# Kernel optimization log

Measured on AMD Instinct MI355X. Metric: run time of the kernel, lower is better.

Reference implementation:

```python
import jax, jax.numpy as jnp
import numpy as np

B, SEQ, DIM, HEADS = 2, 2048, 512, 8
HD = DIM // HEADS
RANK, DFF = 128, 1024
TAU_MEM, TAU_ADAPT, SLOPE, EPS = 0.99, 0.95, 25.0, 1e-6
THRESH, ADAPT_STRENGTH = 0.5, 0.1
TREE_LEVELS = int(np.log2(SEQ))  # 11


def rmsnorm(x, w, eps=EPS):
    return x * jax.lax.rsqrt(jnp.mean(x * x, axis=-1, keepdims=True) + eps) * w


def rope_cos_sin(seq, hd):
    inv = 1.0 / (10000.0 ** (jnp.arange(0, hd, 2, dtype=jnp.float32) / hd))
    f = jnp.arange(seq, dtype=jnp.float32)[:, None] * inv[None, :]  # [S, hd/2]
    emb = jnp.concatenate([f, f], axis=-1)  # [S, hd]
    return jnp.cos(emb), jnp.sin(emb)


def apply_rope(x, cos, sin):
    # x: [B, H, S, hd]; rotate-half formulation
    x1, x2 = jnp.split(x, 2, axis=-1)
    return x * cos + jnp.concatenate([-x2, x1], axis=-1) * sin


def setup_inputs() -> dict:
    key = jax.random.key(0)
    ks = jax.random.split(key, 12)
    w = lambda k, shape, fan: (jax.random.normal(k, shape, jnp.float32) / np.sqrt(fan))
    return {
        "x": jax.random.normal(ks[0], (B, SEQ, DIM), jnp.float32),
        "norm_w": jnp.ones((DIM,), jnp.float32),
        "wq": w(ks[1], (DIM, DIM), DIM),
        "wk": w(ks[2], (DIM, DIM), DIM),
        "wv": w(ks[3], (DIM, DIM), DIM),
        "wo": w(ks[4], (DIM, DIM), DIM),
        "lat_w": w(ks[5], (SEQ, SEQ), SEQ),
        "bt": jnp.full((DIM,), THRESH, jnp.float32),
        "as_w": jnp.full((DIM,), ADAPT_STRENGTH, jnp.float32),
        "gate_w": w(ks[6], (DIM, DIM), DIM),
        "tnorm1_w": jnp.ones((DIM,), jnp.float32),
        "tnorm2_w": jnp.ones((DIM,), jnp.float32),
        "ffn_norm_w": jnp.ones((DIM,), jnp.float32),
        "u_w": w(ks[7], (DIM, RANK), DIM),
        "v_w": w(ks[8], (RANK, 2 * DFF), RANK),
        "down_w": w(ks[9], (DFF, DIM), DFF),
    }


def reference(x, norm_w, wq, wk, wv, wo, lat_w, bt, as_w, gate_w,
              tnorm1_w, tnorm2_w, ffn_norm_w, u_w, v_w, down_w):
    Bx, S, D = x.shape
    # --- pre-norm + QKV projections (base_proj) ---
    h = rmsnorm(x, norm_w)
    q = (h @ wq.T).reshape(Bx, S, HEADS, HD).transpose(0, 2, 1, 3)  # [B,H,S,hd]
    k = (h @ wk.T).reshape(Bx, S, HEADS, HD).transpose(0, 2, 1, 3)
    v = (h @ wv.T).reshape(Bx, S, HEADS, HD).transpose(0, 2, 1, 3)
    # --- RoPE ---
    cos, sin = rope_cos_sin(S, HD)
    q = apply_rope(q, cos, sin)
    k = apply_rope(k, cos, sin)
    # --- causal self-attention ---
    scores = jnp.einsum("bhqd,bhkd->bhqk", q, k) / np.sqrt(HD)
    causal = jnp.tril(jnp.ones((S, S), bool))
    scores = jnp.where(causal, scores, jnp.float32(-1e9))
    attn = jnp.einsum("bhqk,bhkd->bhqd", jax.nn.softmax(scores, axis=-1), v)
    attn = attn.transpose(0, 2, 1, 3).reshape(Bx, S, D) @ wo.T
    # --- causal lateral mixing across sequence ---
    mixed = jnp.einsum("ts,bsd->btd", jnp.tril(lat_w), attn)
    # --- ALIF spiking recurrence over the sequence (soft surrogate spike) ---
    def alif_step(carry, i_t):
        vmem, ad = carry
        vmem = TAU_MEM * vmem + i_t
        th = bt + as_w * ad
        spike = jax.nn.sigmoid(SLOPE * (vmem - th))
        vmem = vmem - spike * th          # soft reset
        ad = TAU_ADAPT * ad + spike        # threshold adaptation
        return (vmem, ad), spike
    init = (jnp.zeros((Bx, D), x.dtype), jnp.zeros((Bx, D), x.dtype))
    _, spikes = jax.lax.scan(alif_step, init, mixed.transpose(1, 0, 2))
    spikes = spikes.transpose(1, 0, 2)  # [B,S,D]
    # --- fused addadd residual ---
    h2 = x + mixed + spikes
    # --- binary-tree cell recursion to a root summary ---
    s = h2
    for _ in range(TREE_LEVELS):
        raw = s[:, 0::2, :] + s[:, 1::2, :]         # pairwise sums (raw_sums)
        res = 0.5 * raw                              # residual / prev_s surrogate
        n = rmsnorm(raw, tnorm1_w)
        g = jax.nn.sigmoid(n @ gate_w.T)
        s = rmsnorm(g * n + (1.0 - g) * res, tnorm2_w)
    h3 = h2 + s[:, 0:1, :]  # broadcast root back over the sequence
    # --- low-rank SwiGLU FFN ---
    hn = rmsnorm(h3, ffn_norm_w)
    up = (hn @ u_w) @ v_w                 # [B,S,2*DFF]
    a, b = jnp.split(up, 2, axis=-1)
    ffn = (jax.nn.silu(a) * b) @ down_w   # [B,S,D]
    return h3 + ffn
```

## Files before the change

### kernel.cpp

```cpp
#include <hip/hip_runtime.h>
#include <math.h>

#define BB 2
#define SS 2048
#define DD 512
#define HH 8
#define HDD 64
#define RANKK 128
#define DFFF 1024

typedef short bf16x8 __attribute__((ext_vector_type(8)));
typedef float f32x4 __attribute__((ext_vector_type(4)));

__device__ __forceinline__ short f2b(float f) {
  union { float f; unsigned u; } v; v.f = f;
  unsigned r = v.u + 0x7FFF + ((v.u >> 16) & 1);
  return (short)(r >> 16);
}
__device__ __forceinline__ float b2f(short s) {
  union { unsigned u; float f; } v; v.u = ((unsigned)(unsigned short)s) << 16;
  return v.f;
}

__device__ __forceinline__ void gll16(const void* g, void* l) {
  __builtin_amdgcn_global_load_lds(
      (const __attribute__((address_space(1))) unsigned int*)g,
      (__attribute__((address_space(3))) unsigned int*)l, 16, 0, 0);
}

__device__ __forceinline__ float wsum(float v) {
#pragma unroll
  for (int off = 32; off > 0; off >>= 1) v += __shfl_xor(v, off, 64);
  return v;
}

__global__ void splitw(const float* __restrict__ in, short* __restrict__ hi,
                       short* __restrict__ lo, int n) {
  int i = (blockIdx.x * 256 + threadIdx.x) * 4;
  if (i >= n) return;
  float4 v = *(const float4*)(in + i);
  short4 h4, l4;
  h4.x = f2b(v.x); l4.x = f2b(v.x - b2f(h4.x));
  h4.y = f2b(v.y); l4.y = f2b(v.y - b2f(h4.y));
  h4.z = f2b(v.z); l4.z = f2b(v.z - b2f(h4.z));
  h4.w = f2b(v.w); l4.w = f2b(v.w - b2f(h4.w));
  *(short4*)(hi + i) = h4;
  *(short4*)(lo + i) = l4;
}

__global__ void cvtb(const float* __restrict__ in, short* __restrict__ out, int n) {
  int i = (blockIdx.x * 256 + threadIdx.x) * 4;
  if (i >= n) return;
  float4 v = *(const float4*)(in + i);
  short4 o; o.x = f2b(v.x); o.y = f2b(v.y); o.z = f2b(v.z); o.w = f2b(v.w);
  *(short4*)(out + i) = o;
}

__global__ void transp_cvt(const float* __restrict__ in, short* __restrict__ out,
                           int R, int C) {
  __shared__ float t[32][33];
  int c0 = blockIdx.x * 32, r0 = blockIdx.y * 32;
#pragma unroll
  for (int i = 0; i < 4; i++) {
    int idx = threadIdx.x + i * 256;
    int r = idx >> 5, c = idx & 31;
    t[r][c] = in[(size_t)(r0 + r) * C + c0 + c];
  }
  __syncthreads();
#pragma unroll
  for (int i = 0; i < 4; i++) {
    int idx = threadIdx.x + i * 256;
    int cc = idx >> 5, rr = idx & 31;
    out[(size_t)(c0 + cc) * R + r0 + rr] = f2b(t[rr][cc]);
  }
}

__global__ void rmsnorm_hl(const float* __restrict__ x, const float* __restrict__ w,
                           short* __restrict__ oh, short* __restrict__ ol, int rows) {
  int wid = blockIdx.x * 4 + (threadIdx.x >> 6);
  int lane = threadIdx.x & 63;
  if (wid >= rows) return;
  const float* xp = x + (size_t)wid * DD + lane * 8;
  float4 a = *(const float4*)xp;
  float4 b = *(const float4*)(xp + 4);
  float ss = a.x*a.x + a.y*a.y + a.z*a.z + a.w*a.w
           + b.x*b.x + b.y*b.y + b.z*b.z + b.w*b.w;
  ss = wsum(ss);
  float r = rsqrtf(ss * (1.0f / DD) + 1e-6f);
  const float* wp = w + lane * 8;
  float4 wa = *(const float4*)wp, wb = *(const float4*)(wp + 4);
  float o8[8] = {a.x*r*wa.x, a.y*r*wa.y, a.z*r*wa.z, a.w*r*wa.w,
                 b.x*r*wb.x, b.y*r*wb.y, b.z*r*wb.z, b.w*r*wb.w};
  short hv[8], lv[8];
#pragma unroll
  for (int i = 0; i < 8; i++) { hv[i] = f2b(o8[i]); lv[i] = f2b(o8[i] - b2f(hv[i])); }
  short* op = oh + (size_t)wid * DD + lane * 8;
  short* lp = ol + (size_t)wid * DD + lane * 8;
  *(short4*)op = make_short4(hv[0], hv[1], hv[2], hv[3]);
  *(short4*)(op + 4) = make_short4(hv[4], hv[5], hv[6], hv[7]);
  *(short4*)lp = make_short4(lv[0], lv[1], lv[2], lv[3]);
  *(short4*)(lp + 4) = make_short4(lv[4], lv[5], lv[6], lv[7]);
}

template <bool SPL, int OM, bool ROPE>
__global__ __launch_bounds__(256) void ggemm(const short* __restrict__ Ah_g,
                                             const short* __restrict__ Al_g,
                                             const short* __restrict__ Bh_g,
                                             const short* __restrict__ Bl_g,
                                             const float* __restrict__ ADD,
                                             void* __restrict__ C, void* __restrict__ C2,
                                             int M, int N, int K) {
  __shared__ short Ahs[128 * 32];
  __shared__ short Bhs[128 * 32];
  __shared__ short Als[SPL ? 128 * 32 : 8];
  __shared__ short Bls[SPL ? 128 * 32 : 8];
  const int tid = threadIdx.x, l = tid & 63, w = tid >> 6;
  const int wr = (w >> 1) * 64, wc = (w & 1) * 64;
  const int bm = blockIdx.y * 128, bn = blockIdx.x * 128;
  f32x4 acc[4][4] = {};
  for (int k0 = 0; k0 < K; k0 += 32) {
#pragma unroll
    for (int p = 0; p < 2; p++) {
      int row = p * 64 + (tid >> 2), g = tid & 3;
      int swz = (g ^ ((row >> 1) & 3)) * 8;
      gll16(Ah_g + (size_t)(bm + row) * K + k0 + swz, Ahs + p * 2048 + tid * 8);
      gll16(Bh_g + (size_t)(bn + row) * K + k0 + swz, Bhs + p * 2048 + tid * 8);
      if (SPL) {
        gll16(Al_g + (size_t)(bm + row) * K + k0 + swz, Als + p * 2048 + tid * 8);
        gll16(Bl_g + (size_t)(bn + row) * K + k0 + swz, Bls + p * 2048 + tid * 8);
      }
    }
    __syncthreads();
    bf16x8 ah[4], bh[4], al[4], bl[4];
#pragma unroll
    for (int m = 0; m < 4; m++) {
      int r = wr + m * 16 + (l & 15);
      int go = (((l >> 4) ^ ((r >> 1) & 3)) << 3);
      ah[m] = *(const bf16x8*)(Ahs + r * 32 + go);
      if (SPL) al[m] = *(const bf16x8*)(Als + r * 32 + go);
    }
#pragma unroll
    for (int n = 0; n < 4; n++) {
      int r = wc + n * 16 + (l & 15);
      int go = (((l >> 4) ^ ((r >> 1) & 3)) << 3);
      bh[n] = *(const bf16x8*)(Bhs + r * 32 + go);
      if (SPL) bl[n] = *(const bf16x8*)(Bls + r * 32 + go);
    }
#pragma unroll
    for (int m = 0; m < 4; m++)
#pragma unroll
      for (int n = 0; n < 4; n++) {
        acc[m][n] = __builtin_amdgcn_mfma_f32_16x16x32_bf16(ah[m], bh[n], acc[m][n], 0, 0, 0);
        if (SPL) {
          acc[m][n] = __builtin_amdgcn_mfma_f32_16x16x32_bf16(ah[m], bl[n], acc[m][n], 0, 0, 0);
          acc[m][n] = __builtin_amdgcn_mfma_f32_16x16x32_bf16(al[m], bh[n], acc[m][n], 0, 0, 0);
        }
      }
    __syncthreads();
  }
  const int ll = l & 15, lg4 = (l >> 4) * 4;
  if (ROPE) {
#pragma unroll
    for (int m = 0; m < 4; m++)
#pragma unroll
      for (int n = 0; n < 2; n++) {
        int i_ = n * 16 + ll;
        float inv = exp2f(-(float)i_ * (13.287712379549449f / 32.0f));
#pragma unroll
        for (int j = 0; j < 4; j++) {
          int gm = bm + wr + m * 16 + lg4 + j;
          int s = gm & (SS - 1);
          float ang = (float)s * inv;
          float sn, cs;
          sincosf(ang, &sn, &cs);
          float v1 = acc[m][n][j], v2 = acc[m][n + 2][j];
          acc[m][n][j]     = v1 * cs - v2 * sn;
          acc[m][n + 2][j] = v2 * cs + v1 * sn;
        }
      }
  }
#pragma unroll
  for (int m = 0; m < 4; m++)
#pragma unroll
    for (int n = 0; n < 4; n++) {
      int gn = bn + wc + n * 16 + ll;
#pragma unroll
      for (int j = 0; j < 4; j++) {
        int gm = bm + wr + m * 16 + lg4 + j;
        if (gm >= M || gn >= N) continue;
        float v = acc[m][n][j];
        if (OM == 0) {
          ((float*)C)[(size_t)gm * N + gn] = v;
        } else if (OM == 1) {
          ((short*)C)[(size_t)gm * N + gn] = f2b(v);
        } else if (OM == 6) {
          size_t off = (size_t)gm * N + gn;
          ((float*)C)[off] = v + ADD[off];
        } else {
          short hi = f2b(v);
          short lo = f2b(v - b2f(hi));
          int b = gm >> 11, s = gm & (SS - 1);
          int hh2 = gn >> 6, d = gn & 63;
          size_t off;
          if (OM == 2)      off = (((size_t)(b * HH + hh2)) * SS + s) * 64 + d;
          else if (OM == 3) off = (((size_t)(b * HH + hh2)) * 64 + d) * SS + s;
          else              off = ((size_t)(b * DD) + gn) * SS + s;
          ((short*)C)[off] = hi;
          ((short*)C2)[off] = lo;
        }
      }
    }
}

__global__ __launch_bounds__(256) void lat_g(const float* __restrict__ lat,
                                             const short* __restrict__ bTh,
                                             const short* __restrict__ bTl,
                                             float* __restrict__ Cc) {
  int z = blockIdx.z;
  bTh += (size_t)z * DD * SS;
  bTl += (size_t)z * DD * SS;
  Cc += (size_t)z * DD * SS;
  __shared__ short Ah[128 * 32];
  __shared__ short Al[128 * 32];
  __shared__ short Bh[128 * 32];
  __shared__ short Bl[128 * 32];
  const int tid = threadIdx.x, l = tid & 63, w = tid >> 6;
  const int wr = (w >> 1) * 64, wc = (w & 1) * 64;
  const int bm = blockIdx.y * 128, bn = blockIdx.x * 128;
  f32x4 acc[4][4] = {};
  const int kend = bm + 128;
  for (int k0 = 0; k0 < kend; k0 += 32) {
#pragma unroll
    for (int p = 0; p < 2; p++) {
      int row = p * 64 + (tid >> 2), g = tid & 3;
      int swz = (g ^ ((row >> 1) & 3)) * 8;
      gll16(bTh + (size_t)(bn + row) * SS + k0 + swz, Bh + p * 2048 + tid * 8);
      gll16(bTl + (size_t)(bn + row) * SS + k0 + swz, Bl + p * 2048 + tid * 8);
    }
#pragma unroll
    for (int i = 0; i < 4; i++) {
      int lin = i * 256 + tid;
      int row = lin >> 3, f4 = lin & 7;
      int gr = bm + row;
      float4 v = *(const float4*)(lat + (size_t)gr * SS + k0 + f4 * 4);
      int kc = k0 + f4 * 4;
      if (kc + 0 > gr) v.x = 0.0f;
      if (kc + 1 > gr) v.y = 0.0f;
      if (kc + 2 > gr) v.z = 0.0f;
      if (kc + 3 > gr) v.w = 0.0f;
      int off = row * 32 + (((f4 >> 1) ^ ((row >> 1) & 3)) << 3) + (f4 & 1) * 4;
      short4 hh, lo;
      hh.x = f2b(v.x); lo.x = f2b(v.x - b2f(hh.x));
      hh.y = f2b(v.y); lo.y = f2b(v.y - b2f(hh.y));
      hh.z = f2b(v.z); lo.z = f2b(v.z - b2f(hh.z));
      hh.w = f2b(v.w); lo.w = f2b(v.w - b2f(hh.w));
      *(short4*)(Ah + off) = hh;
      *(short4*)(Al + off) = lo;
    }
    __syncthreads();
    bf16x8 ah[4], bh[4], al[4], bl[4];
#pragma unroll
    for (int m = 0; m < 4; m++) {
      int r = wr + m * 16 + (l & 15);
      int go = (((l >> 4) ^ ((r >> 1) & 3)) << 3);
      ah[m] = *(const bf16x8*)(Ah + r * 32 + go);
      al[m] = *(const bf16x8*)(Al + r * 32 + go);
    }
#pragma unroll
    for (int n = 0; n < 4; n++) {
      int r = wc + n * 16 + (l & 15);
      int go = (((l >> 4) ^ ((r >> 1) & 3)) << 3);
      bh[n] = *(const bf16x8*)(Bh + r * 32 + go);
      bl[n] = *(const bf16x8*)(Bl + r * 32 + go);
    }
#pragma unroll
    for (int m = 0; m < 4; m++)
#pragma unroll
      for (int n = 0; n < 4; n++) {
        acc[m][n] = __builtin_amdgcn_mfma_f32_16x16x32_bf16(ah[m], bh[n], acc[m][n], 0, 0, 0);
        acc[m][n] = __builtin_amdgcn_mfma_f32_16x16x32_bf16(ah[m], bl[n], acc[m][n], 0, 0, 0);
        acc[m][n] = __builtin_amdgcn_mfma_f32_16x16x32_bf16(al[m], bh[n], acc[m][n], 0, 0, 0);
      }
    __syncthreads();
  }
  const int ll = l & 15, lg4 = (l >> 4) * 4;
#pragma unroll
  for (int m = 0; m < 4; m++)
#pragma unroll
    for (int n = 0; n < 4; n++) {
      int gn = bn + wc + n * 16 + ll;
#pragma unroll
      for (int j = 0; j < 4; j++) {
        int gm = bm + wr + m * 16 + lg4 + j;
        Cc[(size_t)gn * SS + gm] = acc[m][n][j];
      }
    }
}

__global__ __launch_bounds__(256) void attn_g(const short* __restrict__ qh,
                                              const short* __restrict__ ql,
                                              const short* __restrict__ kh,
                                              const short* __restrict__ kl,
                                              const short* __restrict__ vh,
                                              const short* __restrict__ vl,
                                              short* __restrict__ aho,
                                              short* __restrict__ alo) {
  const int h = blockIdx.y, b = blockIdx.z;
  const int qt = (b == 0) ? (int)blockIdx.x : 31 - (int)blockIdx.x;
  const int q0 = qt * 64;
  const int tid = threadIdx.x, w = tid >> 6, l = tid & 63;
  const int lg = l >> 4, ll = l & 15;
  __shared__ short Kh[64 * 64], Kl[64 * 64];
  __shared__ short Vh[64 * 64], Vl[64 * 64];
  __shared__ short Ph[64 * 64], Pl[64 * 64];
  const size_t bh = (size_t)(b * HH + h);

  const int qr = q0 + w * 16 + ll;
  const short* qbh = qh + (bh * SS + qr) * 64;
  const short* qbl = ql + (bh * SS + qr) * 64;
  bf16x8 qfh[2], qfl[2];
#pragma unroll
  for (int ks = 0; ks < 2; ks++) {
    qfh[ks] = *(const bf16x8*)(qbh + (ks * 4 + lg) * 8);
    qfl[ks] = *(const bf16x8*)(qbl + (ks * 4 + lg) * 8);
  }

  f32x4 o[4] = {};
  float mrow[4] = {-1e30f, -1e30f, -1e30f, -1e30f};
  float lsum[4] = {};
  const int qrow0 = q0 + w * 16 + lg * 4;
  const int ntiles = qt + 1;

  for (int kt = 0; kt < ntiles; kt++) {
#pragma unroll
    for (int p = 0; p < 2; p++) {
      int row = p * 32 + (tid >> 3), g = tid & 7;
      int sw = ((g ^ (row & 7)) << 3);
      size_t krow = (bh * SS + kt * 64 + row) * 64;
      size_t vrow = (bh * 64 + row) * SS + kt * 64;
      gll16(kh + krow + sw, Kh + p * 2048 + tid * 8);
      gll16(kl + krow + sw, Kl + p * 2048 + tid * 8);
      gll16(vh + vrow + sw, Vh + p * 2048 + tid * 8);
      gll16(vl + vrow + sw, Vl + p * 2048 + tid * 8);
    }
    __syncthreads();

    f32x4 sv[4] = {};
#pragma unroll
    for (int nf = 0; nf < 4; nf++) {
      int r = nf * 16 + ll;
#pragma unroll
      for (int ks = 0; ks < 2; ks++) {
        int g = (ks * 4 + lg) ^ (r & 7);
        bf16x8 khf = *(const bf16x8*)(Kh + r * 64 + g * 8);
        bf16x8 klf = *(const bf16x8*)(Kl + r * 64 + g * 8);
        sv[nf] = __builtin_amdgcn_mfma_f32_16x16x32_bf16(qfh[ks], khf, sv[nf], 0, 0, 0);
        sv[nf] = __builtin_amdgcn_mfma_f32_16x16x32_bf16(qfh[ks], klf, sv[nf], 0, 0, 0);
        sv[nf] = __builtin_amdgcn_mfma_f32_16x16x32_bf16(qfl[ks], khf, sv[nf], 0, 0, 0);
      }
    }
#pragma unroll
    for (int nf = 0; nf < 4; nf++) {
      int kpos = kt * 64 + nf * 16 + ll;
#pragma unroll
      for (int j = 0; j < 4; j++) {
        float v = sv[nf][j] * 0.125f;
        sv[nf][j] = (kpos > qrow0 + j) ? -1e30f : v;
      }
    }
    float cf[4];
#pragma unroll
    for (int j = 0; j < 4; j++) {
      float r = fmaxf(fmaxf(sv[0][j], sv[1][j]), fmaxf(sv[2][j], sv[3][j]));
      r = fmaxf(r, __shfl_xor(r, 1)); r = fmaxf(r, __shfl_xor(r, 2));
      r = fmaxf(r, __shfl_xor(r, 4)); r = fmaxf(r, __shfl_xor(r, 8));
      float mn = fmaxf(mrow[j], r);
      cf[j] = __expf(mrow[j] - mn);
      mrow[j] = mn;
    }
    float ps[4] = {};
#pragma unroll
    for (int nf = 0; nf < 4; nf++)
#pragma unroll
      for (int j = 0; j < 4; j++) {
        float p = __expf(sv[nf][j] - mrow[j]);
        sv[nf][j] = p;
        ps[j] += p;
      }
#pragma unroll
    for (int j = 0; j < 4; j++) {
      float r = ps[j];
      r += __shfl_xor(r, 1); r += __shfl_xor(r, 2);
      r += __shfl_xor(r, 4); r += __shfl_xor(r, 8);
      lsum[j] = lsum[j] * cf[j] + r;
    }
#pragma unroll
    for (int nf = 0; nf < 4; nf++)
#pragma unroll
      for (int j = 0; j < 4; j++) o[nf][j] *= cf[j];
#pragma unroll
    for (int nf = 0; nf < 4; nf++)
#pragma unroll
      for (int j = 0; j < 4; j++) {
        int rowP = w * 16 + lg * 4 + j;
        int col = nf * 16 + ll;
        int off = rowP * 64 + (((col >> 3) ^ (rowP & 7)) << 3) + (col & 7);
        float p = sv[nf][j];
        short hi = f2b(p);
        Ph[off] = hi;
        Pl[off] = f2b(p - b2f(hi));
      }
    __syncthreads();
    bf16x8 pfh[2], pfl[2];
    {
      int rowA = w * 16 + ll;
#pragma unroll
      for (int ks = 0; ks < 2; ks++) {
        int g = (ks * 4 + lg) ^ (rowA & 7);
        pfh[ks] = *(const bf16x8*)(Ph + rowA * 64 + g * 8);
        pfl[ks] = *(const bf16x8*)(Pl + rowA * 64 + g * 8);
      }
    }
#pragma unroll
    for (int nf = 0; nf < 4; nf++) {
      int r = nf * 16 + ll;
#pragma unroll
      for (int ks = 0; ks < 2; ks++) {
        int g = (ks * 4 + lg) ^ (r & 7);
        bf16x8 vhf = *(const bf16x8*)(Vh + r * 64 + g * 8);
        bf16x8 vlf = *(const bf16x8*)(Vl + r * 64 + g * 8);
        o[nf] = __builtin_amdgcn_mfma_f32_16x16x32_bf16(pfh[ks], vhf, o[nf], 0, 0, 0);
        o[nf] = __builtin_amdgcn_mfma_f32_16x16x32_bf16(pfh[ks], vlf, o[nf], 0, 0, 0);
        o[nf] = __builtin_amdgcn_mfma_f32_16x16x32_bf16(pfl[ks], vhf, o[nf], 0, 0, 0);
      }
    }
    __syncthreads();
  }
  float inv[4];
#pragma unroll
  for (int j = 0; j < 4; j++) inv[j] = 1.0f / lsum[j];
#pragma unroll
  for (int nf = 0; nf < 4; nf++)
#pragma unroll
    for (int j = 0; j < 4; j++) {
      float v = o[nf][j] * inv[j];
      short hi = f2b(v);
      size_t off = ((size_t)(b * SS + qrow0 + j)) * DD + h * HDD + nf * 16 + ll;
      aho[off] = hi;
      alo[off] = f2b(v - b2f(hi));
    }
}

#define ACH 32
__global__ __launch_bounds__(64) void tsa_alif4(const float* __restrict__ mixedT,
                                                const float* __restrict__ bt,
                                                const float* __restrict__ asw,
                                                float* __restrict__ spikesT) {
  int tid = blockIdx.x * 64 + threadIdx.x;
  int b = tid >> 9, d = tid & 511;
  const float btd = bt[d], asd = asw[d];
  const float C = 36.06737602222409f;
  const float bt36 = btd * C, as36 = asd * C;
  const float bt99 = 0.99f * btd, as99 = 0.99f * asd;
  const float* mp = mixedT + ((size_t)(b * DD + d)) * SS;
  float* sp = spikesT + ((size_t)(b * DD + d)) * SS;
  float mA[ACH], mB[ACH], sO[ACH];
#pragma unroll
  for (int k = 0; k < ACH / 4; k++) *(float4*)&mA[k * 4] = *(const float4*)(mp + k * 4);
#pragma unroll
  for (int k = 0; k < ACH / 4; k++) *(float4*)&mB[k * 4] = *(const float4*)(mp + ACH + k * 4);
  float vR = mA[0];
  float ad = 0.0f;
  for (int t0 = 0; t0 < SS; t0 += 2 * ACH) {
    bool more = (t0 + 2 * ACH < SS);
#pragma unroll
    for (int j = 0; j < ACH; j++) {
      float thC = fmaf(ad, as36, bt36);
      float th99 = fmaf(ad, as99, bt99);
      float arg = fmaf(vR, -C, thC);
      float e = exp2f(arg);
      float s = __builtin_amdgcn_rcpf(1.0f + e);
      float mn = (j + 1 < ACH) ? mA[j + 1] : mB[0];
      float pre = fmaf(0.99f, vR, mn);
      sO[j] = s;
      vR = fmaf(-th99, s, pre);
      ad = fmaf(0.95f, ad, s);
    }
#pragma unroll
    for (int k = 0; k < ACH / 4; k++) *(float4*)(sp + t0 + k * 4) = *(const float4*)&sO[k * 4];
    if (more) {
#pragma unroll
      for (int k = 0; k < ACH / 4; k++)
        *(float4*)&mA[k * 4] = *(const float4*)(mp + t0 + 2 * ACH + k * 4);
    }
#pragma unroll
    for (int j = 0; j < ACH; j++) {
      float thC = fmaf(ad, as36, bt36);
      float th99 = fmaf(ad, as99, bt99);
      float arg = fmaf(vR, -C, thC);
      float e = exp2f(arg);
      float s = __builtin_amdgcn_rcpf(1.0f + e);
      float mn = (j + 1 < ACH) ? mB[j + 1] : (more ? mA[0] : 0.0f);
      float pre = fmaf(0.99f, vR, mn);
      sO[j] = s;
      vR = fmaf(-th99, s, pre);
      ad = fmaf(0.95f, ad, s);
    }
#pragma unroll
    for (int k = 0; k < ACH / 4; k++) *(float4*)(sp + t0 + ACH + k * 4) = *(const float4*)&sO[k * 4];
    if (more) {
#pragma unroll
      for (int k = 0; k < ACH / 4; k++)
        *(float4*)&mB[k * 4] = *(const float4*)(mp + t0 + 3 * ACH + k * 4);
    }
  }
}

__global__ __launch_bounds__(256) void fuse_h2(const float* __restrict__ x,
                                               const float* __restrict__ mixedT,
                                               const float* __restrict__ spikesT,
                                               float* __restrict__ h2) {
  const int s0 = blockIdx.x * 64, d0 = blockIdx.y * 64, b = blockIdx.z;
  __shared__ float t[64][65];
#pragma unroll
  for (int k = 0; k < 4; k++) {
    int dl = threadIdx.x >> 2;
    int sl = (threadIdx.x & 3) * 16 + k * 4;
    size_t off = ((size_t)(b * DD + d0 + dl)) * SS + s0 + sl;
    float4 mv = *(const float4*)(mixedT + off);
    float4 sv = *(const float4*)(spikesT + off);
    t[dl][sl + 0] = mv.x + sv.x;
    t[dl][sl + 1] = mv.y + sv.y;
    t[dl][sl + 2] = mv.z + sv.z;
    t[dl][sl + 3] = mv.w + sv.w;
  }
  __syncthreads();
#pragma unroll
  for (int k = 0; k < 4; k++) {
    int sl = threadIdx.x >> 2;
    int dl = (threadIdx.x & 3) * 16 + k * 4;
    size_t off = ((size_t)(b * SS + s0 + sl)) * DD + d0 + dl;
    float4 xv = *(const float4*)(x + off);
    float4 o;
    o.x = xv.x + t[dl + 0][sl];
    o.y = xv.y + t[dl + 1][sl];
    o.z = xv.z + t[dl + 2][sl];
    o.w = xv.w + t[dl + 3][sl];
    *(float4*)(h2 + off) = o;
  }
}

__global__ void tree_reduce_b(const float* __restrict__ sin_, const float* __restrict__ tn1,
                              short* __restrict__ nb, int Sn) {
  int wid = blockIdx.x * 4 + (threadIdx.x >> 6);
  int lane = threadIdx.x & 63;
  int rows = BB * Sn;
  if (wid >= rows) return;
  int b = wid / Sn, j = wid - b * Sn;
  const float* r0 = sin_ + ((size_t)(b * 2 * Sn + 2 * j)) * DD + lane * 8;
  const float* r1 = r0 + DD;
  float4 a0 = *(const float4*)r0, a1 = *(const float4*)(r0 + 4);
  float4 b0 = *(const float4*)r1, b1 = *(const float4*)(r1 + 4);
  float ra[8] = {a0.x + b0.x, a0.y + b0.y, a0.z + b0.z, a0.w + b0.w,
                 a1.x + b1.x, a1.y + b1.y, a1.z + b1.z, a1.w + b1.w};
  float ss = 0.0f;
#pragma unroll
  for (int i = 0; i < 8; i++) ss += ra[i] * ra[i];
  ss = wsum(ss);
  float rms = rsqrtf(ss * (1.0f / DD) + 1e-6f);
  const float* wp = tn1 + lane * 8;
  float4 wa = *(const float4*)wp, wb = *(const float4*)(wp + 4);
  float wv8[8] = {wa.x, wa.y, wa.z, wa.w, wb.x, wb.y, wb.z, wb.w};
  short* np = nb + (size_t)wid * DD + lane * 8;
  short4 n0, n1;
  n0.x = f2b(ra[0]*rms*wv8[0]); n0.y = f2b(ra[1]*rms*wv8[1]);
  n0.z = f2b(ra[2]*rms*wv8[2]); n0.w = f2b(ra[3]*rms*wv8[3]);
  n1.x = f2b(ra[4]*rms*wv8[4]); n1.y = f2b(ra[5]*rms*wv8[5]);
  n1.z = f2b(ra[6]*rms*wv8[6]); n1.w = f2b(ra[7]*rms*wv8[7]);
  *(short4*)np = n0;
  *(short4*)(np + 4) = n1;
}

__global__ void tree_combine_b(const float* __restrict__ g, const short* __restrict__ nb,
                               const float* __restrict__ sin_, const float* __restrict__ tn2,
                               float* __restrict__ sout, int Sn) {
  int wid = blockIdx.x * 4 + (threadIdx.x >> 6);
  int lane = threadIdx.x & 63;
  int rows = BB * Sn;
  if (wid >= rows) return;
  int b = wid / Sn, j = wid - b * Sn;
  const float* r0 = sin_ + ((size_t)(b * 2 * Sn + 2 * j)) * DD + lane * 8;
  const float* r1 = r0 + DD;
  float4 a0 = *(const float4*)r0, a1 = *(const float4*)(r0 + 4);
  float4 b0 = *(const float4*)r1, b1 = *(const float4*)(r1 + 4);
  float res[8] = {0.5f*(a0.x + b0.x), 0.5f*(a0.y + b0.y), 0.5f*(a0.z + b0.z), 0.5f*(a0.w + b0.w),
                  0.5f*(a1.x + b1.x), 0.5f*(a1.y + b1.y), 0.5f*(a1.z + b1.z), 0.5f*(a1.w + b1.w)};
  size_t base = (size_t)wid * DD + lane * 8;
  float t[8];
  float ss = 0.0f;
#pragma unroll
  for (int i = 0; i < 8; i++) {
    float gg = 1.0f / (1.0f + expf(-g[base + i]));
    float tv = gg * b2f(nb[base + i]) + (1.0f - gg) * res[i];
    t[i] = tv;
    ss += tv * tv;
  }
  ss = wsum(ss);
  float rms = rsqrtf(ss * (1.0f / DD) + 1e-6f);
#pragma unroll
  for (int i = 0; i < 8; i++) sout[base + i] = t[i] * rms * tn2[lane * 8 + i];
}

__global__ void h3hn_b(const float* __restrict__ h2, const float* __restrict__ root,
                       const float* __restrict__ fw, float* __restrict__ h3,
                       short* __restrict__ hn) {
  int wid = blockIdx.x * 4 + (threadIdx.x >> 6);
  int lane = threadIdx.x & 63;
  int b = wid >> 11;
  size_t base = (size_t)wid * DD + lane * 8;
  const float* rp = root + (size_t)b * DD + lane * 8;
  float t[8];
  float ss = 0.0f;
#pragma unroll
  for (int i = 0; i < 8; i++) {
    float tv = h2[base + i] + rp[i];
    t[i] = tv;
    ss += tv * tv;
    h3[base + i] = tv;
  }
  ss = wsum(ss);
  float rms = rsqrtf(ss * (1.0f / DD) + 1e-6f);
#pragma unroll
  for (int i = 0; i < 8; i++) hn[base + i] = f2b(t[i] * rms * fw[lane * 8 + i]);
}

__global__ __launch_bounds__(256) void upgate_g(const short* __restrict__ A,
                                                const short* __restrict__ Bv,
                                                short* __restrict__ ffa) {
  __shared__ short Ahs[128 * 32];
  __shared__ short B1s[128 * 32];
  __shared__ short B2s[128 * 32];
  const int tid = threadIdx.x, l = tid & 63, w = tid >> 6;
  const int wr = (w >> 1) * 64, wc = (w & 1) * 64;
  const int bm = blockIdx.y * 128, bn = blockIdx.x * 128;
  f32x4 acc1[4][4] = {}, acc2[4][4] = {};
  for (int k0 = 0; k0 < RANKK; k0 += 32) {
#pragma unroll
    for (int p = 0; p < 2; p++) {
      int row = p * 64 + (tid >> 2), g = tid & 3;
      int swz = (g ^ ((row >> 1) & 3)) * 8;
      gll16(A + (size_t)(bm + row) * RANKK + k0 + swz, Ahs + p * 2048 + tid * 8);
      gll16(Bv + (size_t)(bn + row) * RANKK + k0 + swz, B1s + p * 2048 + tid * 8);
      gll16(Bv + (size_t)(DFFF + bn + row) * RANKK + k0 + swz, B2s + p * 2048 + tid * 8);
    }
    __syncthreads();
    bf16x8 ah[4], b1[4], b2[4];
#pragma unroll
    for (int m = 0; m < 4; m++) {
      int r = wr + m * 16 + (l & 15);
      int go = (((l >> 4) ^ ((r >> 1) & 3)) << 3);
      ah[m] = *(const bf16x8*)(Ahs + r * 32 + go);
    }
#pragma unroll
    for (int n = 0; n < 4; n++) {
      int r = wc + n * 16 + (l & 15);
      int go = (((l >> 4) ^ ((r >> 1) & 3)) << 3);
      b1[n] = *(const bf16x8*)(B1s + r * 32 + go);
      b2[n] = *(const bf16x8*)(B2s + r * 32 + go);
    }
#pragma unroll
    for (int m = 0; m < 4; m++)
#pragma unroll
      for (int n = 0; n < 4; n++) {
        acc1[m][n] = __builtin_amdgcn_mfma_f32_16x16x32_bf16(ah[m], b1[n], acc1[m][n], 0, 0, 0);
        acc2[m][n] = __builtin_amdgcn_mfma_f32_16x16x32_bf16(ah[m], b2[n], acc2[m][n], 0, 0, 0);
      }
    __syncthreads();
  }
#pragma unroll
  for (int m = 0; m < 4; m++)
#pragma unroll
    for (int n = 0; n < 4; n++) {
      int gn = bn + wc + n * 16 + (l & 15);
#pragma unroll
      for (int j = 0; j < 4; j++) {
        int gm = bm + wr + m * 16 + (l >> 4) * 4 + j;
        float a = acc1[m][n][j];
        float s = a / (1.0f + __expf(-a));
        ffa[(size_t)gm * DFFF + gn] = f2b(s * acc2[m][n][j]);
      }
    }
}

extern "C" void kernel_launch(void* const* d_in, const int* in_sizes, int n_in,
                              void* d_out, int out_size, void* d_ws, size_t ws_size,
                              hipStream_t stream) {
  const float* x   = (const float*)d_in[0];
  const float* nw  = (const float*)d_in[1];
  const float* wq  = (const float*)d_in[2];
  const float* wk  = (const float*)d_in[3];
  const float* wv  = (const float*)d_in[4];
  const float* wo  = (const float*)d_in[5];
  const float* lat = (const float*)d_in[6];
  const float* btp = (const float*)d_in[7];
  const float* asw = (const float*)d_in[8];
  const float* gw  = (const float*)d_in[9];
  const float* tn1 = (const float*)d_in[10];
  const float* tn2 = (const float*)d_in[11];
  const float* fnw = (const float*)d_in[12];
  const float* uw  = (const float*)d_in[13];
  const float* vw  = (const float*)d_in[14];
  const float* dw  = (const float*)d_in[15];
  float* out = (float*)d_out;
  char* W = (char*)d_ws;
  const size_t MB = 1u << 20;

  short* h_hi = (short*)(W);
  short* h_lo = (short*)(W + 4 * MB);
  short* attn_hi = h_hi;
  short* attn_lo = h_lo;
  short* nb = (short*)(W);
  float* gb = (float*)(W + 2 * MB);
  short* q_hi = (short*)(W + 8 * MB);
  short* q_lo = (short*)(W + 12 * MB);
  short* apT_hi = q_hi;
  short* apT_lo = q_lo;
  float* spikesT = (float*)(W + 8 * MB);
  float* s0 = (float*)(W + 8 * MB);
  float* s1 = (float*)(W + 12 * MB);
  short* k_hi = (short*)(W + 16 * MB);
  short* k_lo = (short*)(W + 20 * MB);
  short* hn = (short*)(W + 16 * MB);
  short* t1 = (short*)(W + 20 * MB);
  short* v_hi = (short*)(W + 24 * MB);
  short* v_lo = (short*)(W + 28 * MB);
  float* h2 = (float*)(W + 24 * MB);
  short* ffa = (short*)(W + 24 * MB);
  float* mixedT = (float*)(W + 32 * MB);
  short* gwb = (short*)(W + 32 * MB);
  short* uwT = gwb + 262144;
  short* vwT = uwT + 65536;
  short* dwT = vwT + 262144;

  short* wqh = (short*)out;
  short* wql = wqh + 262144;
  short* wkh = wql + 262144;
  short* wkl = wkh + 262144;
  short* wvh = wkl + 262144;
  short* wvl = wvh + 262144;
  short* woh = wvl + 262144;
  short* wol = woh + 262144;

  const int rows = BB * SS;

  splitw<<<256, 256, 0, stream>>>(wq, wqh, wql, DD * DD);
  splitw<<<256, 256, 0, stream>>>(wk, wkh, wkl, DD * DD);
  splitw<<<256, 256, 0, stream>>>(wv, wvh, wvl, DD * DD);
  splitw<<<256, 256, 0, stream>>>(wo, woh, wol, DD * DD);

  rmsnorm_hl<<<rows / 4, 256, 0, stream>>>(x, nw, h_hi, h_lo, rows);

  ggemm<true, 2, true><<<dim3(4, 32), 256, 0, stream>>>(
      h_hi, h_lo, wqh, wql, nullptr, q_hi, q_lo, rows, DD, DD);
  ggemm<true, 2, true><<<dim3(4, 32), 256, 0, stream>>>(
      h_hi, h_lo, wkh, wkl, nullptr, k_hi, k_lo, rows, DD, DD);
  ggemm<true, 3, false><<<dim3(4, 32), 256, 0, stream>>>(
      h_hi, h_lo, wvh, wvl, nullptr, v_hi, v_lo, rows, DD, DD);

  attn_g<<<dim3(32, HH, BB), 256, 0, stream>>>(q_hi, q_lo, k_hi, k_lo, v_hi, v_lo,
                                               attn_hi, attn_lo);

  ggemm<true, 4, false><<<dim3(4, 32), 256, 0, stream>>>(
      attn_hi, attn_lo, woh, wol, nullptr, apT_hi, apT_lo, rows, DD, DD);

  lat_g<<<dim3(4, 16, 2), 256, 0, stream>>>(lat, apT_hi, apT_lo, mixedT);

  tsa_alif4<<<16, 64, 0, stream>>>(mixedT, btp, asw, spikesT);
  fuse_h2<<<dim3(32, 8, 2), 256, 0, stream>>>(x, mixedT, spikesT, h2);

  cvtb<<<256, 256, 0, stream>>>(gw, gwb, DD * DD);
  transp_cvt<<<dim3(4, 16), 256, 0, stream>>>(uw, uwT, DD, RANKK);
  transp_cvt<<<dim3(64, 4), 256, 0, stream>>>(vw, vwT, RANKK, 2 * DFFF);
  transp_cvt<<<dim3(16, 32), 256, 0, stream>>>(dw, dwT, DFFF, DD);

  const float* sin_ = h2;
  for (int lvl = 0; lvl < 11; lvl++) {
    int Sn = 1024 >> lvl;
    int r2 = BB * Sn;
    float* sout = (lvl & 1) ? s1 : s0;
    tree_reduce_b<<<(r2 + 3) / 4, 256, 0, stream>>>(sin_, tn1, nb, Sn);
    ggemm<false, 0, false><<<dim3(4, (r2 + 127) / 128), 256, 0, stream>>>(
        nb, nullptr, gwb, nullptr, nullptr, gb, nullptr, r2, DD, DD);
    tree_combine_b<<<(r2 + 3) / 4, 256, 0, stream>>>(gb, nb, sin_, tn2, sout, Sn);
    sin_ = sout;
  }

  h3hn_b<<<rows / 4, 256, 0, stream>>>(h2, sin_, fnw, out, hn);

  ggemm<false, 1, false><<<dim3(1, 32), 256, 0, stream>>>(
      hn, nullptr, uwT, nullptr, nullptr, t1, nullptr, rows, RANKK, DD);
  upgate_g<<<dim3(8, 32), 256, 0, stream>>>(t1, vwT, ffa);
  ggemm<false, 6, false><<<dim3(4, 32), 256, 0, stream>>>(
      ffa, nullptr, dwT, nullptr, out, out, nullptr, rows, DD, DFFF);
}
```

Baseline: 771.8 us.

## Fuse QKV GEMMs into one launch and split causal lateral GEMM over K

Replaces the three separate Q, K and V projection GEMM launches with one batched kernel over blockIdx.z, with RoPE applied in the epilogue. The causal lateral-mixing GEMM is split along K into two halves that write separate partial buffers, which doubles the block count and shortens the longest blocks in the triangular workload. The scan and fuse_h2 kernels now read and sum both partials, adding memory traffic and an extra workspace buffer in exchange for better load balance and fewer launches.

```diff
diff --git a/kernel.cpp b/kernel.cpp
--- a/kernel.cpp
+++ b/kernel.cpp
@@ -212,14 +212,116 @@
     }
 }
 
+__global__ __launch_bounds__(256) void qkv_g(const short* __restrict__ Ah_g,
+                                             const short* __restrict__ Al_g,
+                                             const short* __restrict__ wh0, const short* __restrict__ wl0,
+                                             const short* __restrict__ wh1, const short* __restrict__ wl1,
+                                             const short* __restrict__ wh2, const short* __restrict__ wl2,
+                                             short* __restrict__ c0h, short* __restrict__ c0l,
+                                             short* __restrict__ c1h, short* __restrict__ c1l,
+                                             short* __restrict__ c2h, short* __restrict__ c2l) {
+  const int z = blockIdx.z;
+  const short* Bh_g = (z == 0) ? wh0 : (z == 1) ? wh1 : wh2;
+  const short* Bl_g = (z == 0) ? wl0 : (z == 1) ? wl1 : wl2;
+  short* Ch = (z == 0) ? c0h : (z == 1) ? c1h : c2h;
+  short* Cl = (z == 0) ? c0l : (z == 1) ? c1l : c2l;
+  const int K = DD;
+  __shared__ short Ahs[128 * 32];
+  __shared__ short Bhs[128 * 32];
+  __shared__ short Als[128 * 32];
+  __shared__ short Bls[128 * 32];
+  const int tid = threadIdx.x, l = tid & 63, w = tid >> 6;
+  const int wr = (w >> 1) * 64, wc = (w & 1) * 64;
+  const int bm = blockIdx.y * 128, bn = blockIdx.x * 128;
+  f32x4 acc[4][4] = {};
+  for (int k0 = 0; k0 < K; k0 += 32) {
+#pragma unroll
+    for (int p = 0; p < 2; p++) {
+      int row = p * 64 + (tid >> 2), g = tid & 3;
+      int swz = (g ^ ((row >> 1) & 3)) * 8;
+      gll16(Ah_g + (size_t)(bm + row) * K + k0 + swz, Ahs + p * 2048 + tid * 8);
+      gll16(Bh_g + (size_t)(bn + row) * K + k0 + swz, Bhs + p * 2048 + tid * 8);
+      gll16(Al_g + (size_t)(bm + row) * K + k0 + swz, Als + p * 2048 + tid * 8);
+      gll16(Bl_g + (size_t)(bn + row) * K + k0 + swz, Bls + p * 2048 + tid * 8);
+    }
+    __syncthreads();
+    bf16x8 ah[4], bh[4], al[4], bl[4];
+#pragma unroll
+    for (int m = 0; m < 4; m++) {
+      int r = wr + m * 16 + (l & 15);
+      int go = (((l >> 4) ^ ((r >> 1) & 3)) << 3);
+      ah[m] = *(const bf16x8*)(Ahs + r * 32 + go);
+      al[m] = *(const bf16x8*)(Als + r * 32 + go);
+    }
+#pragma unroll
+    for (int n = 0; n < 4; n++) {
+      int r = wc + n * 16 + (l & 15);
+      int go = (((l >> 4) ^ ((r >> 1) & 3)) << 3);
+      bh[n] = *(const bf16x8*)(Bhs + r * 32 + go);
+      bl[n] = *(const bf16x8*)(Bls + r * 32 + go);
+    }
+#pragma unroll
+    for (int m = 0; m < 4; m++)
+#pragma unroll
+      for (int n = 0; n < 4; n++) {
+        acc[m][n] = __builtin_amdgcn_mfma_f32_16x16x32_bf16(ah[m], bh[n], acc[m][n], 0, 0, 0);
+        acc[m][n] = __builtin_amdgcn_mfma_f32_16x16x32_bf16(ah[m], bl[n], acc[m][n], 0, 0, 0);
+        acc[m][n] = __builtin_amdgcn_mfma_f32_16x16x32_bf16(al[m], bh[n], acc[m][n], 0, 0, 0);
+      }
+    __syncthreads();
+  }
+  const int ll = l & 15, lg4 = (l >> 4) * 4;
+  if (z < 2) {
+#pragma unroll
+    for (int m = 0; m < 4; m++)
+#pragma unroll
+      for (int n = 0; n < 2; n++) {
+        int i_ = n * 16 + ll;
+        float inv = exp2f(-(float)i_ * (13.287712379549449f / 32.0f));
+#pragma unroll
+        for (int j = 0; j < 4; j++) {
+          int gm = bm + wr + m * 16 + lg4 + j;
+          int s = gm & (SS - 1);
+          float ang = (float)s * inv;
+          float sn, cs;
+          sincosf(ang, &sn, &cs);
+          float v1 = acc[m][n][j], v2 = acc[m][n + 2][j];
+          acc[m][n][j]     = v1 * cs - v2 * sn;
+          acc[m][n + 2][j] = v2 * cs + v1 * sn;
+        }
+      }
+  }
+#pragma unroll
+  for (int m = 0; m < 4; m++)
+#pragma unroll
+    for (int n = 0; n < 4; n++) {
+      int gn = bn + wc + n * 16 + ll;
+#pragma unroll
+      for (int j = 0; j < 4; j++) {
+        int gm = bm + wr + m * 16 + lg4 + j;
+        float v = acc[m][n][j];
+        short hi = f2b(v);
+        short lo = f2b(v - b2f(hi));
+        int b = gm >> 11, s = gm & (SS - 1);
+        int hh2 = gn >> 6, d = gn & 63;
+        size_t off = (z < 2) ? ((((size_t)(b * HH + hh2)) * SS + s) * 64 + d)
+                             : ((((size_t)(b * HH + hh2)) * 64 + d) * SS + s);
+        Ch[off] = hi;
+        Cl[off] = lo;
+      }
+    }
+}
+
 __global__ __launch_bounds__(256) void lat_g(const float* __restrict__ lat,
                                              const short* __restrict__ bTh,
                                              const short* __restrict__ bTl,
-                                             float* __restrict__ Cc) {
-  int z = blockIdx.z;
-  bTh += (size_t)z * DD * SS;
-  bTl += (size_t)z * DD * SS;
-  Cc += (size_t)z * DD * SS;
+                                             float* __restrict__ P0,
+                                             float* __restrict__ P1) {
+  const int zb = blockIdx.z >> 1;
+  const int half = blockIdx.z & 1;
+  bTh += (size_t)zb * DD * SS;
+  bTl += (size_t)zb * DD * SS;
+  float* Cc = (half == 0 ? P0 : P1) + (size_t)zb * DD * SS;
   __shared__ short Ah[128 * 32];
   __shared__ short Al[128 * 32];
   __shared__ short Bh[128 * 32];
@@ -227,9 +329,13 @@
   const int tid = threadIdx.x, l = tid & 63, w = tid >> 6;
   const int wr = (w >> 1) * 64, wc = (w & 1) * 64;
   const int bm = blockIdx.y * 128, bn = blockIdx.x * 128;
+  const int T = blockIdx.y + 1;
+  const int h0 = (T + 1) >> 1;
+  const int kbeg = (half == 0) ? 0 : h0 * 128;
+  const int kend = (half == 0) ? h0 * 128 : T * 128;
   f32x4 acc[4][4] = {};
-  const int kend = bm + 128;
-  for (int k0 = 0; k0 < kend; k0 += 32) {
+  const int ll = l & 15, lg4 = (l >> 4) * 4;
+  for (int k0 = kbeg; k0 < kend; k0 += 32) {
 #pragma unroll
     for (int p = 0; p < 2; p++) {
       int row = p * 64 + (tid >> 2), g = tid & 3;
@@ -283,7 +389,6 @@
       }
     __syncthreads();
   }
-  const int ll = l & 15, lg4 = (l >> 4) * 4;
 #pragma unroll
   for (int m = 0; m < 4; m++)
 #pragma unroll
@@ -452,7 +557,8 @@
 }
 
 #define ACH 32
-__global__ __launch_bounds__(64) void tsa_alif4(const float* __restrict__ mixedT,
+__global__ __launch_bounds__(64) void tsa_alif4(const float* __restrict__ P0,
+                                                const float* __restrict__ P1,
                                                 const float* __restrict__ bt,
                                                 const float* __restrict__ asw,
                                                 float* __restrict__ spikesT) {
@@ -462,13 +568,25 @@
   const float C = 36.06737602222409f;
   const float bt36 = btd * C, as36 = asd * C;
   const float bt99 = 0.99f * btd, as99 = 0.99f * asd;
-  const float* mp = mixedT + ((size_t)(b * DD + d)) * SS;
-  float* sp = spikesT + ((size_t)(b * DD + d)) * SS;
+  const size_t base = ((size_t)(b * DD + d)) * SS;
+  const float* p0 = P0 + base;
+  const float* p1 = P1 + base;
+  float* sp = spikesT + base;
   float mA[ACH], mB[ACH], sO[ACH];
 #pragma unroll
-  for (int k = 0; k < ACH / 4; k++) *(float4*)&mA[k * 4] = *(const float4*)(mp + k * 4);
-#pragma unroll
-  for (int k = 0; k < ACH / 4; k++) *(float4*)&mB[k * 4] = *(const float4*)(mp + ACH + k * 4);
+  for (int k = 0; k < ACH / 4; k++) {
+    float4 a = *(const float4*)(p0 + k * 4);
+    float4 bq = *(const float4*)(p1 + k * 4);
+    mA[k*4+0] = a.x + bq.x; mA[k*4+1] = a.y + bq.y;
+    mA[k*4+2] = a.z + bq.z; mA[k*4+3] = a.w + bq.w;
+  }
+#pragma unroll
+  for (int k = 0; k < ACH / 4; k++) {
+    float4 a = *(const float4*)(p0 + ACH + k * 4);
+    float4 bq = *(const float4*)(p1 + ACH + k * 4);
+    mB[k*4+0] = a.x + bq.x; mB[k*4+1] = a.y + bq.y;
+    mB[k*4+2] = a.z + bq.z; mB[k*4+3] = a.w + bq.w;
+  }
   float vR = mA[0];
   float ad = 0.0f;
   for (int t0 = 0; t0 < SS; t0 += 2 * ACH) {
@@ -490,8 +608,12 @@
     for (int k = 0; k < ACH / 4; k++) *(float4*)(sp + t0 + k * 4) = *(const float4*)&sO[k * 4];
     if (more) {
 #pragma unroll
-      for (int k = 0; k < ACH / 4; k++)
-        *(float4*)&mA[k * 4] = *(const float4*)(mp + t0 + 2 * ACH + k * 4);
+      for (int k = 0; k < ACH / 4; k++) {
+        float4 a = *(const float4*)(p0 + t0 + 2 * ACH + k * 4);
+        float4 bq = *(const float4*)(p1 + t0 + 2 * ACH + k * 4);
+        mA[k*4+0] = a.x + bq.x; mA[k*4+1] = a.y + bq.y;
+        mA[k*4+2] = a.z + bq.z; mA[k*4+3] = a.w + bq.w;
+      }
     }
 #pragma unroll
     for (int j = 0; j < ACH; j++) {
@@ -510,14 +632,19 @@
     for (int k = 0; k < ACH / 4; k++) *(float4*)(sp + t0 + ACH + k * 4) = *(const float4*)&sO[k * 4];
     if (more) {
 #pragma unroll
-      for (int k = 0; k < ACH / 4; k++)
-        *(float4*)&mB[k * 4] = *(const float4*)(mp + t0 + 3 * ACH + k * 4);
+      for (int k = 0; k < ACH / 4; k++) {
+        float4 a = *(const float4*)(p0 + t0 + 3 * ACH + k * 4);
+        float4 bq = *(const float4*)(p1 + t0 + 3 * ACH + k * 4);
+        mB[k*4+0] = a.x + bq.x; mB[k*4+1] = a.y + bq.y;
+        mB[k*4+2] = a.z + bq.z; mB[k*4+3] = a.w + bq.w;
+      }
     }
   }
 }
 
 __global__ __launch_bounds__(256) void fuse_h2(const float* __restrict__ x,
-                                               const float* __restrict__ mixedT,
+                                               const float* __restrict__ P0,
+                                               const float* __restrict__ P1,
                                                const float* __restrict__ spikesT,
                                                float* __restrict__ h2) {
   const int s0 = blockIdx.x * 64, d0 = blockIdx.y * 64, b = blockIdx.z;
@@ -527,12 +654,13 @@
     int dl = threadIdx.x >> 2;
     int sl = (threadIdx.x & 3) * 16 + k * 4;
     size_t off = ((size_t)(b * DD + d0 + dl)) * SS + s0 + sl;
-    float4 mv = *(const float4*)(mixedT + off);
+    float4 m0 = *(const float4*)(P0 + off);
+    float4 m1 = *(const float4*)(P1 + off);
     float4 sv = *(const float4*)(spikesT + off);
-    t[dl][sl + 0] = mv.x + sv.x;
-    t[dl][sl + 1] = mv.y + sv.y;
-    t[dl][sl + 2] = mv.z + sv.z;
-    t[dl][sl + 3] = mv.w + sv.w;
+    t[dl][sl + 0] = m0.x + m1.x + sv.x;
+    t[dl][sl + 1] = m0.y + m1.y + sv.y;
+    t[dl][sl + 2] = m0.z + m1.z + sv.z;
+    t[dl][sl + 3] = m0.w + m1.w + sv.w;
   }
   __syncthreads();
 #pragma unroll
@@ -730,13 +858,14 @@
   float* s1 = (float*)(W + 12 * MB);
   short* k_hi = (short*)(W + 16 * MB);
   short* k_lo = (short*)(W + 20 * MB);
+  float* latP1 = (float*)(W + 16 * MB);
   short* hn = (short*)(W + 16 * MB);
   short* t1 = (short*)(W + 20 * MB);
   short* v_hi = (short*)(W + 24 * MB);
   short* v_lo = (short*)(W + 28 * MB);
   float* h2 = (float*)(W + 24 * MB);
   short* ffa = (short*)(W + 24 * MB);
-  float* mixedT = (float*)(W + 32 * MB);
+  float* latP0 = (float*)(W + 32 * MB);
   short* gwb = (short*)(W + 32 * MB);
   short* uwT = gwb + 262144;
   short* vwT = uwT + 65536;
@@ -760,12 +889,9 @@
 
   rmsnorm_hl<<<rows / 4, 256, 0, stream>>>(x, nw, h_hi, h_lo, rows);
 
-  ggemm<true, 2, true><<<dim3(4, 32), 256, 0, stream>>>(
-      h_hi, h_lo, wqh, wql, nullptr, q_hi, q_lo, rows, DD, DD);
-  ggemm<true, 2, true><<<dim3(4, 32), 256, 0, stream>>>(
-      h_hi, h_lo, wkh, wkl, nullptr, k_hi, k_lo, rows, DD, DD);
-  ggemm<true, 3, false><<<dim3(4, 32), 256, 0, stream>>>(
-      h_hi, h_lo, wvh, wvl, nullptr, v_hi, v_lo, rows, DD, DD);
+  qkv_g<<<dim3(4, 32, 3), 256, 0, stream>>>(h_hi, h_lo,
+                                            wqh, wql, wkh, wkl, wvh, wvl,
+                                            q_hi, q_lo, k_hi, k_lo, v_hi, v_lo);
 
   attn_g<<<dim3(32, HH, BB), 256, 0, stream>>>(q_hi, q_lo, k_hi, k_lo, v_hi, v_lo,
                                                attn_hi, attn_lo);
@@ -773,10 +899,10 @@
   ggemm<true, 4, false><<<dim3(4, 32), 256, 0, stream>>>(
       attn_hi, attn_lo, woh, wol, nullptr, apT_hi, apT_lo, rows, DD, DD);
 
-  lat_g<<<dim3(4, 16, 2), 256, 0, stream>>>(lat, apT_hi, apT_lo, mixedT);
-
-  tsa_alif4<<<16, 64, 0, stream>>>(mixedT, btp, asw, spikesT);
-  fuse_h2<<<dim3(32, 8, 2), 256, 0, stream>>>(x, mixedT, spikesT, h2);
+  lat_g<<<dim3(4, 16, 4), 256, 0, stream>>>(lat, apT_hi, apT_lo, latP0, latP1);
+
+  tsa_alif4<<<16, 64, 0, stream>>>(latP0, latP1, btp, asw, spikesT);
+  fuse_h2<<<dim3(32, 8, 2), 256, 0, stream>>>(x, latP0, latP1, spikesT, h2);
 
   cvtb<<<256, 256, 0, stream>>>(gw, gwb, DD * DD);
   transp_cvt<<<dim3(4, 16), 256, 0, stream>>>(uw, uwT, DD, RANKK);
```

Result: faster. 693.9 us (-10.1%).
